# Kernel tuning notes

Hardware: AMD Instinct MI355X
Metric: run time of the kernel (lower is better)

Reference implementation:

```python
import jax, jax.numpy as jnp
import numpy as np

B, LQ, LKV, D, H = 4, 1024, 4096, 512, 4
HD = D // H  # head dim = 128


def setup_inputs() -> dict:
    key = jax.random.key(0)
    ks = jax.random.split(key, 6)
    s = 1.0 / np.sqrt(D)
    return {
        "x": jax.random.normal(ks[0], (B, LQ, D), jnp.float32),
        "encoder_feats": jax.random.normal(ks[1], (B, LKV, D), jnp.float32),
        "Wq": jax.random.normal(ks[2], (D, D), jnp.float32) * s,
        "Wk": jax.random.normal(ks[3], (D, D), jnp.float32) * s,
        "Wv": jax.random.normal(ks[4], (D, D), jnp.float32) * s,
        "bq": jnp.zeros((D,), jnp.float32),
        "bk": jnp.zeros((D,), jnp.float32),
        "bv": jnp.zeros((D,), jnp.float32),
        "Wo": jax.random.normal(ks[5], (D, D), jnp.float32) * s,
        "bo": jnp.zeros((D,), jnp.float32),
    }


def reference(x, encoder_feats, Wq, Wk, Wv, bq, bk, bv, Wo, bo):
    # nn.MultiheadAttention explicit (non-flash) path, dropout=0, eval.
    # Project, split heads: [B, L, D] -> [B, H, L, HD]
    def heads(t, L):
        return t.reshape(B, L, H, HD).transpose(0, 2, 1, 3)

    q = heads(x @ Wq.T + bq, LQ)
    k = heads(encoder_feats @ Wk.T + bk, LKV)
    v = heads(encoder_feats @ Wv.T + bv, LKV)

    scale = 1.0 / jnp.sqrt(jnp.asarray(HD, x.dtype))
    scores = jnp.einsum("bhqd,bhkd->bhqk", q, k) * scale  # [B,H,LQ,LKV]
    attn = jax.nn.softmax(scores, axis=-1)
    ctx = jnp.einsum("bhqk,bhkd->bhqd", attn, v)  # [B,H,LQ,HD]
    ctx = ctx.transpose(0, 2, 1, 3).reshape(B, LQ, D)
    attn_output = ctx @ Wo.T + bo
    # forward() returns attn_output only (fused/LayerNorm result is discarded)
    return attn_output
```

## Files before the change

kernel.cpp:

```cpp
#include <hip/hip_runtime.h>
#include <math.h>

#define B_    4
#define LQ_   1024
#define LKV_  4096
#define DM    512
#define NH    4
#define HD_   128

typedef _Float16 half8   __attribute__((ext_vector_type(8)));
typedef _Float16 half4_t __attribute__((ext_vector_type(4)));
typedef float    floatx4 __attribute__((ext_vector_type(4)));

#define MFMA16(a, b, c) __builtin_amdgcn_mfma_f32_16x16x32_f16((a), (b), (c), 0, 0, 0)

#define SWZ(c, r) ((c) ^ (((r) & 7) << 3))

__global__ __launch_bounds__(256) void prep_w(
    const float* __restrict__ Wq, const float* __restrict__ Wk,
    const float* __restrict__ Wv, const float* __restrict__ Wo,
    _Float16* __restrict__ Wh)
{
  int i = blockIdx.x * 256 + threadIdx.x;
  int wsel = i >> 16;
  const float* src = (wsel == 0) ? Wq : (wsel == 1) ? Wk : (wsel == 2) ? Wv : Wo;
  size_t off = i & 65535;
  float4 v = *(const float4*)(src + off * 4);
  half4_t h;
  h[0] = (_Float16)v.x; h[1] = (_Float16)v.y;
  h[2] = (_Float16)v.z; h[3] = (_Float16)v.w;
  *(half4_t*)(Wh + ((size_t)wsel << 18) + off * 4) = h;
}

__global__ __launch_bounds__(256, 2) void proj_qkv(
    const float* __restrict__ x,
    const float* __restrict__ enc,
    const _Float16* __restrict__ Whq,
    const _Float16* __restrict__ Whk,
    const _Float16* __restrict__ Whv,
    const float* __restrict__ bq,
    const float* __restrict__ bk,
    const float* __restrict__ bv,
    _Float16* __restrict__ Qh,
    _Float16* __restrict__ Kh,
    _Float16* __restrict__ Vt,
    float qscale)
{
  __shared__ _Float16 SM[3 * 128 * 72];
  _Float16 (*Xs)[72]  = (_Float16(*)[72])SM;
  _Float16 (*Ws1)[72] = (_Float16(*)[72])(SM + 128 * 72);
  _Float16 (*Ws2)[72] = (_Float16(*)[72])(SM + 2 * 128 * 72);

  const int tid  = threadIdx.x;
  const int lane = tid & 63;
  const int w    = tid >> 6;
  const int n16  = lane & 15;
  const int quad = lane >> 4;
  const int wm   = (w & 1) * 64;
  const int wn   = (w >> 1) * 64;
  const int col0 = blockIdx.y * 128;

  if ((int)blockIdx.x >= 128) {
    const int row0 = ((int)blockIdx.x - 128) * 128;
    floatx4 acc[4][4];
#pragma unroll
    for (int a = 0; a < 4; ++a)
#pragma unroll
      for (int b = 0; b < 4; ++b) acc[a][b] = (floatx4){0.f, 0.f, 0.f, 0.f};

    for (int k0 = 0; k0 < 512; k0 += 64) {
#pragma unroll
      for (int i = 0; i < 4; ++i) {
        int c = i * 256 + tid;
        int r = c >> 3, off = (c & 7) * 8;
        const float* xp = x + (size_t)(row0 + r) * 512 + k0 + off;
        float4 a = *(const float4*)xp, b2 = *(const float4*)(xp + 4);
        half8 hx;
        hx[0] = (_Float16)a.x;  hx[1] = (_Float16)a.y;
        hx[2] = (_Float16)a.z;  hx[3] = (_Float16)a.w;
        hx[4] = (_Float16)b2.x; hx[5] = (_Float16)b2.y;
        hx[6] = (_Float16)b2.z; hx[7] = (_Float16)b2.w;
        *(half8*)&Xs[r][off] = hx;
        *(half8*)&Ws1[r][off] = *(const half8*)(Whq + (size_t)(col0 + r) * 512 + k0 + off);
      }
      __syncthreads();
#pragma unroll
      for (int kc = 0; kc < 2; ++kc) {
        half8 af[4], bf[4];
#pragma unroll
        for (int mb = 0; mb < 4; ++mb)
          af[mb] = *(const half8*)&Xs[wm + mb * 16 + n16][kc * 32 + quad * 8];
#pragma unroll
        for (int nb = 0; nb < 4; ++nb)
          bf[nb] = *(const half8*)&Ws1[wn + nb * 16 + n16][kc * 32 + quad * 8];
#pragma unroll
        for (int mb = 0; mb < 4; ++mb)
#pragma unroll
          for (int nb = 0; nb < 4; ++nb)
            acc[mb][nb] = MFMA16(af[mb], bf[nb], acc[mb][nb]);
      }
      __syncthreads();
    }
#pragma unroll
    for (int mb = 0; mb < 4; ++mb)
#pragma unroll
      for (int nb = 0; nb < 4; ++nb)
#pragma unroll
        for (int r = 0; r < 4; ++r) {
          int row = row0 + wm + mb * 16 + quad * 4 + r;
          int col = col0 + wn + nb * 16 + n16;
          Qh[(size_t)row * 512 + col] =
              (_Float16)((acc[mb][nb][r] + bq[col]) * qscale);
        }
    return;
  }

  const int row0 = (int)blockIdx.x * 128;
  floatx4 accK[4][4], accV[4][4];
#pragma unroll
  for (int a = 0; a < 4; ++a)
#pragma unroll
    for (int b = 0; b < 4; ++b) {
      accK[a][b] = (floatx4){0.f, 0.f, 0.f, 0.f};
      accV[a][b] = (floatx4){0.f, 0.f, 0.f, 0.f};
    }

  for (int k0 = 0; k0 < 512; k0 += 64) {
#pragma unroll
    for (int i = 0; i < 4; ++i) {
      int c = i * 256 + tid;
      int r = c >> 3, off = (c & 7) * 8;
      const float* xp = enc + (size_t)(row0 + r) * 512 + k0 + off;
      float4 a = *(const float4*)xp, b2 = *(const float4*)(xp + 4);
      half8 hx;
      hx[0] = (_Float16)a.x;  hx[1] = (_Float16)a.y;
      hx[2] = (_Float16)a.z;  hx[3] = (_Float16)a.w;
      hx[4] = (_Float16)b2.x; hx[5] = (_Float16)b2.y;
      hx[6] = (_Float16)b2.z; hx[7] = (_Float16)b2.w;
      *(half8*)&Xs[r][off] = hx;
      *(half8*)&Ws1[r][off] = *(const half8*)(Whk + (size_t)(col0 + r) * 512 + k0 + off);
      *(half8*)&Ws2[r][off] = *(const half8*)(Whv + (size_t)(col0 + r) * 512 + k0 + off);
    }
    __syncthreads();
#pragma unroll
    for (int kc = 0; kc < 2; ++kc) {
      half8 af[4], bkf[4], bvf[4];
#pragma unroll
      for (int mb = 0; mb < 4; ++mb)
        af[mb] = *(const half8*)&Xs[wm + mb * 16 + n16][kc * 32 + quad * 8];
#pragma unroll
      for (int nb = 0; nb < 4; ++nb) {
        bkf[nb] = *(const half8*)&Ws1[wn + nb * 16 + n16][kc * 32 + quad * 8];
        bvf[nb] = *(const half8*)&Ws2[wn + nb * 16 + n16][kc * 32 + quad * 8];
      }
#pragma unroll
      for (int mb = 0; mb < 4; ++mb)
#pragma unroll
        for (int nb = 0; nb < 4; ++nb) {
          accK[mb][nb] = MFMA16(af[mb], bkf[nb], accK[mb][nb]);
          accV[mb][nb] = MFMA16(af[mb], bvf[nb], accV[mb][nb]);
        }
    }
    __syncthreads();
  }

#pragma unroll
  for (int mb = 0; mb < 4; ++mb)
#pragma unroll
    for (int nb = 0; nb < 4; ++nb)
#pragma unroll
      for (int r = 0; r < 4; ++r) {
        int row = row0 + wm + mb * 16 + quad * 4 + r;
        int col = col0 + wn + nb * 16 + n16;
        Kh[(size_t)row * 512 + col] = (_Float16)(accK[mb][nb][r] + bk[col]);
      }

  _Float16 (*Ts)[144] = (_Float16(*)[144])SM;
#pragma unroll
  for (int mb = 0; mb < 4; ++mb)
#pragma unroll
    for (int nb = 0; nb < 4; ++nb) {
      int dl = wn + nb * 16 + n16;
      float bi = bv[col0 + dl];
      half4_t hv;
#pragma unroll
      for (int r = 0; r < 4; ++r) hv[r] = (_Float16)(accV[mb][nb][r] + bi);
      *(half4_t*)&Ts[dl][wm + mb * 16 + quad * 4] = hv;
    }
  __syncthreads();
  int b   = row0 >> 12;
  int kv0 = row0 & 4095;
#pragma unroll
  for (int i = 0; i < 8; ++i) {
    int f = i * 256 + tid;
    int dl = f >> 4, kv8 = (f & 15) * 8;
    half8 ov = *(const half8*)&Ts[dl][kv8];
    *(half8*)(Vt + (size_t)((b * 4 + blockIdx.y) * 128 + dl) * LKV_ + kv0 + kv8) = ov;
  }
}

__global__ __launch_bounds__(256, 2) void flash_mfma2(
    const _Float16* __restrict__ Qh,
    const _Float16* __restrict__ Kh,
    const _Float16* __restrict__ Vtg,
    _Float16* __restrict__ Opart,
    float* __restrict__ ml)
{
  __shared__ _Float16 U[64 * 128];
  __shared__ _Float16 Vs[128 * 64];
  _Float16* Ks = U;
  _Float16* Ps = U;

  const int tid  = threadIdx.x;
  const int lane = tid & 63;
  const int w    = tid >> 6;
  const int n16  = lane & 15;
  const int quad = lane >> 4;

  const int xb    = blockIdx.x;
  const int qt    = blockIdx.y;
  const int split = xb & 3;
  const int bh    = xb >> 2;
  const int h = bh & 3, b = bh >> 2;

  const _Float16* Qg = Qh + (size_t)(b * LQ_ + qt * 128) * DM + h * HD_;
  const _Float16* Kg = Kh + (size_t)(b * LKV_) * DM + h * HD_;
  const _Float16* Vg = Vtg + (size_t)(bh * HD_) * LKV_;

  half8 qf[2][4];
  const int chunk = w >> 1;
  const int qrb   = (w & 1) * 32;
#pragma unroll
  for (int c = 0; c < 2; ++c) {
#pragma unroll
    for (int i = 0; i < 4; ++i) {
      int f = i * 256 + tid;
      int r = f >> 4, c8 = (f & 15) * 8;
      *(half8*)&Ks[r * 128 + SWZ(c8, r)] =
          *(const half8*)(Qg + (size_t)(c * 64 + r) * DM + c8);
    }
    __syncthreads();
    if (chunk == c) {
#pragma unroll
      for (int qb = 0; qb < 2; ++qb) {
        int qr = qrb + qb * 16 + n16;
#pragma unroll
        for (int kc = 0; kc < 4; ++kc)
          qf[qb][kc] = *(const half8*)&Ks[qr * 128 + SWZ(kc * 32 + quad * 8, qr)];
      }
    }
    __syncthreads();
  }

  floatx4 o[2][8];
#pragma unroll
  for (int mb = 0; mb < 2; ++mb)
#pragma unroll
    for (int vb = 0; vb < 8; ++vb) o[mb][vb] = (floatx4){0.f, 0.f, 0.f, 0.f};
  float m_i[2] = {-INFINITY, -INFINITY};
  float l_i[2] = {0.f, 0.f};

  for (int kt = split * 16; kt < split * 16 + 16; ++kt) {
#pragma unroll
    for (int i = 0; i < 4; ++i) {
      int f = i * 256 + tid;
      int r = f >> 4, c8 = (f & 15) * 8;
      *(half8*)&Ks[r * 128 + SWZ(c8, r)] =
          *(const half8*)(Kg + (size_t)(kt * 64 + r) * DM + c8);
    }
#pragma unroll
    for (int i = 0; i < 4; ++i) {
      int f = i * 256 + tid;
      int d = f >> 3, kv8 = (f & 7) * 8;
      *(half8*)&Vs[d * 64 + SWZ(kv8, d)] =
          *(const half8*)(Vg + (size_t)d * LKV_ + kt * 64 + kv8);
    }
    __syncthreads();

    floatx4 s[2][4];
#pragma unroll
    for (int qb = 0; qb < 2; ++qb)
#pragma unroll
      for (int cb = 0; cb < 4; ++cb) s[qb][cb] = (floatx4){0.f, 0.f, 0.f, 0.f};
#pragma unroll
    for (int cb = 0; cb < 4; ++cb) {
      int kr = cb * 16 + n16;
#pragma unroll
      for (int kc = 0; kc < 4; ++kc) {
        half8 kf = *(const half8*)&Ks[kr * 128 + SWZ(kc * 32 + quad * 8, kr)];
        s[0][cb] = MFMA16(kf, qf[0][kc], s[0][cb]);
        s[1][cb] = MFMA16(kf, qf[1][kc], s[1][cb]);
      }
    }
    __syncthreads();

    float alpha[2];
#pragma unroll
    for (int qb = 0; qb < 2; ++qb) {
      float mx = -INFINITY;
#pragma unroll
      for (int cb = 0; cb < 4; ++cb)
#pragma unroll
        for (int r = 0; r < 4; ++r) mx = fmaxf(mx, s[qb][cb][r]);
      mx = fmaxf(mx, __shfl_xor(mx, 16));
      mx = fmaxf(mx, __shfl_xor(mx, 32));
      float mn = fmaxf(m_i[qb], mx);
      alpha[qb] = __expf(m_i[qb] - mn);
      m_i[qb] = mn;
      float rs = 0.f;
      int pr = w * 32 + qb * 16 + n16;
#pragma unroll
      for (int cb = 0; cb < 4; ++cb) {
        half4_t ph;
#pragma unroll
        for (int r = 0; r < 4; ++r) {
          float p = __expf(s[qb][cb][r] - mn);
          rs += p;
          ph[r] = (_Float16)p;
        }
        *(half4_t*)&Ps[pr * 64 + SWZ(cb * 16 + quad * 4, pr)] = ph;
      }
      rs += __shfl_xor(rs, 16);
      rs += __shfl_xor(rs, 32);
      l_i[qb] = l_i[qb] * alpha[qb] + rs;
    }

    if (__ballot((alpha[0] != 1.f) || (alpha[1] != 1.f))) {
#pragma unroll
      for (int mb = 0; mb < 2; ++mb) {
#pragma unroll
        for (int r = 0; r < 4; ++r) {
          float a = __shfl(alpha[mb], (lane & 48) | (quad * 4 + r));
#pragma unroll
          for (int vb = 0; vb < 8; ++vb) o[mb][vb][r] *= a;
        }
      }
    }

    half8 pf[2][2];
#pragma unroll
    for (int mb = 0; mb < 2; ++mb) {
      int pr = w * 32 + mb * 16 + n16;
#pragma unroll
      for (int kc = 0; kc < 2; ++kc)
        pf[mb][kc] = *(const half8*)&Ps[pr * 64 + SWZ(kc * 32 + quad * 8, pr)];
    }
#pragma unroll
    for (int vb = 0; vb < 8; ++vb) {
      int vr = vb * 16 + n16;
#pragma unroll
      for (int kc = 0; kc < 2; ++kc) {
        half8 vf = *(const half8*)&Vs[vr * 64 + SWZ(kc * 32 + quad * 8, vr)];
        o[0][vb] = MFMA16(pf[0][kc], vf, o[0][vb]);
        o[1][vb] = MFMA16(pf[1][kc], vf, o[1][vb]);
      }
    }
    __syncthreads();
  }

  _Float16* Og = Opart + ((size_t)xb * 1024 + qt * 128 + w * 32) * HD_;
#pragma unroll
  for (int mb = 0; mb < 2; ++mb)
#pragma unroll
    for (int r = 0; r < 4; ++r)
#pragma unroll
      for (int vb = 0; vb < 8; ++vb)
        Og[(size_t)(mb * 16 + quad * 4 + r) * HD_ + vb * 16 + n16] =
            (_Float16)o[mb][vb][r];
  if (quad == 0) {
#pragma unroll
    for (int qb = 0; qb < 2; ++qb) {
      size_t qi = (size_t)xb * 1024 + qt * 128 + w * 32 + qb * 16 + n16;
      ml[qi * 2] = m_i[qb];
      ml[qi * 2 + 1] = l_i[qb];
    }
  }
}

__global__ __launch_bounds__(256) void proj_out_fused(
    const _Float16* __restrict__ Opart,
    const float* __restrict__ ml,
    const _Float16* __restrict__ Who,
    const float* __restrict__ bo,
    float* __restrict__ Y)
{
  __shared__ _Float16 Xs[64][72];
  __shared__ _Float16 Ws[128][72];
  __shared__ float CW[4][64][8];

  const int tid  = threadIdx.x;
  const int lane = tid & 63;
  const int w    = tid >> 6;
  const int n16  = lane & 15;
  const int quad = lane >> 4;
  const int wm   = (w & 1) * 32;
  const int wn   = (w >> 1) * 64;
  const int row0 = blockIdx.x * 64;
  const int col0 = blockIdx.y * 128;
  const int b    = row0 >> 10;

  {
    int h = tid >> 6, r = tid & 63;
    int q = (row0 + r) & 1023;
    int bh = b * 4 + h;
    float m[4], l[4], M = -INFINITY;
#pragma unroll
    for (int p = 0; p < 4; ++p) {
      size_t idx = ((size_t)(bh * 4 + p) * 1024 + q) * 2;
      m[p] = ml[idx]; l[p] = ml[idx + 1];
      M = fmaxf(M, m[p]);
    }
    float L = 0.f, wts[4];
#pragma unroll
    for (int p = 0; p < 4; ++p) { wts[p] = __expf(m[p] - M); L += wts[p] * l[p]; }
    float inv = 1.f / L;
#pragma unroll
    for (int p = 0; p < 4; ++p) CW[h][r][p] = wts[p] * inv;
    CW[h][r][4] = 0.f;
  }
  __syncthreads();

  floatx4 acc[2][4];
#pragma unroll
  for (int a = 0; a < 2; ++a)
#pragma unroll
    for (int c = 0; c < 4; ++c) acc[a][c] = (floatx4){0.f, 0.f, 0.f, 0.f};

  for (int k0 = 0; k0 < 512; k0 += 64) {
    int h = k0 >> 7, d0 = k0 & 127;
    int bh = b * 4 + h;
#pragma unroll
    for (int i = 0; i < 2; ++i) {
      int f = i * 256 + tid;
      int r = f >> 3, c8 = (f & 7) * 8;
      int q = (row0 + r) & 1023;
      float w0 = CW[h][r][0], w1 = CW[h][r][1];
      float w2 = CW[h][r][2], w3 = CW[h][r][3];
      size_t base = ((size_t)(bh * 4) * 1024 + q) * 128 + d0 + c8;
      half8 v0 = *(const half8*)(Opart + base);
      half8 v1 = *(const half8*)(Opart + base + 131072);
      half8 v2 = *(const half8*)(Opart + base + 262144);
      half8 v3 = *(const half8*)(Opart + base + 393216);
      half8 hx;
#pragma unroll
      for (int j = 0; j < 8; ++j)
        hx[j] = (_Float16)(w0 * (float)v0[j] + w1 * (float)v1[j] +
                           w2 * (float)v2[j] + w3 * (float)v3[j]);
      *(half8*)&Xs[r][c8] = hx;
    }
#pragma unroll
    for (int i = 0; i < 4; ++i) {
      int f = i * 256 + tid;
      int r = f >> 3, c8 = (f & 7) * 8;
      *(half8*)&Ws[r][c8] = *(const half8*)(Who + (size_t)(col0 + r) * 512 + k0 + c8);
    }
    __syncthreads();
#pragma unroll
    for (int kc = 0; kc < 2; ++kc) {
      half8 af[2], bf[4];
#pragma unroll
      for (int mb = 0; mb < 2; ++mb)
        af[mb] = *(const half8*)&Xs[wm + mb * 16 + n16][kc * 32 + quad * 8];
#pragma unroll
      for (int nb = 0; nb < 4; ++nb)
        bf[nb] = *(const half8*)&Ws[wn + nb * 16 + n16][kc * 32 + quad * 8];
#pragma unroll
      for (int mb = 0; mb < 2; ++mb)
#pragma unroll
        for (int nb = 0; nb < 4; ++nb)
          acc[mb][nb] = MFMA16(af[mb], bf[nb], acc[mb][nb]);
    }
    __syncthreads();
  }

#pragma unroll
  for (int mb = 0; mb < 2; ++mb)
#pragma unroll
    for (int nb = 0; nb < 4; ++nb)
#pragma unroll
      for (int r = 0; r < 4; ++r) {
        int row = row0 + wm + mb * 16 + quad * 4 + r;
        int col = col0 + wn + nb * 16 + n16;
        Y[(size_t)row * 512 + col] = acc[mb][nb][r] + bo[col];
      }
}

extern "C" void kernel_launch(void* const* d_in, const int* in_sizes, int n_in,
                              void* d_out, int out_size, void* d_ws, size_t ws_size,
                              hipStream_t stream) {
  const float* x   = (const float*)d_in[0];
  const float* enc = (const float*)d_in[1];
  const float* Wq  = (const float*)d_in[2];
  const float* Wk  = (const float*)d_in[3];
  const float* Wv  = (const float*)d_in[4];
  const float* bq  = (const float*)d_in[5];
  const float* bk  = (const float*)d_in[6];
  const float* bv  = (const float*)d_in[7];
  const float* Wo  = (const float*)d_in[8];
  const float* bo  = (const float*)d_in[9];
  float* out = (float*)d_out;

  char* ws = (char*)d_ws;
  _Float16* Qh    = (_Float16*)(ws);
  _Float16* Kh    = (_Float16*)(ws + (4u  << 20));
  _Float16* Vtg   = (_Float16*)(ws + (20u << 20));
  _Float16* Opart = (_Float16*)(ws + (36u << 20));
  float*    mlp   = (float*)   (ws + (52u << 20));
  _Float16* Wh    = (_Float16*)(ws + (53u << 20));

  _Float16* Whq = Wh;
  _Float16* Whk = Wh + 262144;
  _Float16* Whv = Wh + 524288;
  _Float16* Who = Wh + 786432;

  const float qscale = 0.08838834764831845f;
  dim3 blk(256);

  prep_w<<<dim3(1024), blk, 0, stream>>>(Wq, Wk, Wv, Wo, Wh);

  proj_qkv<<<dim3(160, 4), blk, 0, stream>>>(
      x, enc, Whq, Whk, Whv, bq, bk, bv, Qh, Kh, Vtg, qscale);

  flash_mfma2<<<dim3(64, 8), blk, 0, stream>>>(Qh, Kh, Vtg, Opart, mlp);

  proj_out_fused<<<dim3(64, 4), blk, 0, stream>>>(Opart, mlp, Who, bo, out);
}
```

Before: 205.8 us.

## Swizzle GEMM shared tiles and transpose flash PV accumulator for coalesced stores

Replaces the padded 72-wide shared tiles in the projection and output GEMM kernels with unpadded 64-wide tiles using XOR swizzle, cutting LDS footprint while still avoiding bank conflicts. In the flash kernel the PV MFMA operands are swapped so the accumulator is held transposed; the alpha rescale then becomes a plain per-lane multiply with no shuffles. The output is staged through shared memory and written with coalesced 16-byte stores instead of scattered 2-byte stores. The staging adds an extra barrier and LDS round trip at the end of the flash kernel.

New measurement: 193.5 us. -6.0%, faster.

```diff
diff --git a/kernel.cpp b/kernel.cpp
--- a/kernel.cpp
+++ b/kernel.cpp
@@ -46,10 +46,10 @@
     _Float16* __restrict__ Vt,
     float qscale)
 {
-  __shared__ _Float16 SM[3 * 128 * 72];
-  _Float16 (*Xs)[72]  = (_Float16(*)[72])SM;
-  _Float16 (*Ws1)[72] = (_Float16(*)[72])(SM + 128 * 72);
-  _Float16 (*Ws2)[72] = (_Float16(*)[72])(SM + 2 * 128 * 72);
+  __shared__ _Float16 SM[3 * 128 * 64];
+  _Float16* Xs  = SM;
+  _Float16* Ws1 = SM + 128 * 64;
+  _Float16* Ws2 = SM + 2 * 128 * 64;
 
   const int tid  = threadIdx.x;
   const int lane = tid & 63;
@@ -80,19 +80,24 @@
         hx[2] = (_Float16)a.z;  hx[3] = (_Float16)a.w;
         hx[4] = (_Float16)b2.x; hx[5] = (_Float16)b2.y;
         hx[6] = (_Float16)b2.z; hx[7] = (_Float16)b2.w;
-        *(half8*)&Xs[r][off] = hx;
-        *(half8*)&Ws1[r][off] = *(const half8*)(Whq + (size_t)(col0 + r) * 512 + k0 + off);
+        *(half8*)&Xs[r * 64 + SWZ(off, r)] = hx;
+        *(half8*)&Ws1[r * 64 + SWZ(off, r)] =
+            *(const half8*)(Whq + (size_t)(col0 + r) * 512 + k0 + off);
       }
       __syncthreads();
 #pragma unroll
       for (int kc = 0; kc < 2; ++kc) {
         half8 af[4], bf[4];
 #pragma unroll
-        for (int mb = 0; mb < 4; ++mb)
-          af[mb] = *(const half8*)&Xs[wm + mb * 16 + n16][kc * 32 + quad * 8];
-#pragma unroll
-        for (int nb = 0; nb < 4; ++nb)
-          bf[nb] = *(const half8*)&Ws1[wn + nb * 16 + n16][kc * 32 + quad * 8];
+        for (int mb = 0; mb < 4; ++mb) {
+          int r = wm + mb * 16 + n16;
+          af[mb] = *(const half8*)&Xs[r * 64 + SWZ(kc * 32 + quad * 8, r)];
+        }
+#pragma unroll
+        for (int nb = 0; nb < 4; ++nb) {
+          int r = wn + nb * 16 + n16;
+          bf[nb] = *(const half8*)&Ws1[r * 64 + SWZ(kc * 32 + quad * 8, r)];
+        }
 #pragma unroll
         for (int mb = 0; mb < 4; ++mb)
 #pragma unroll
@@ -137,21 +142,26 @@
       hx[2] = (_Float16)a.z;  hx[3] = (_Float16)a.w;
       hx[4] = (_Float16)b2.x; hx[5] = (_Float16)b2.y;
       hx[6] = (_Float16)b2.z; hx[7] = (_Float16)b2.w;
-      *(half8*)&Xs[r][off] = hx;
-      *(half8*)&Ws1[r][off] = *(const half8*)(Whk + (size_t)(col0 + r) * 512 + k0 + off);
-      *(half8*)&Ws2[r][off] = *(const half8*)(Whv + (size_t)(col0 + r) * 512 + k0 + off);
+      *(half8*)&Xs[r * 64 + SWZ(off, r)] = hx;
+      *(half8*)&Ws1[r * 64 + SWZ(off, r)] =
+          *(const half8*)(Whk + (size_t)(col0 + r) * 512 + k0 + off);
+      *(half8*)&Ws2[r * 64 + SWZ(off, r)] =
+          *(const half8*)(Whv + (size_t)(col0 + r) * 512 + k0 + off);
     }
     __syncthreads();
 #pragma unroll
     for (int kc = 0; kc < 2; ++kc) {
       half8 af[4], bkf[4], bvf[4];
 #pragma unroll
-      for (int mb = 0; mb < 4; ++mb)
-        af[mb] = *(const half8*)&Xs[wm + mb * 16 + n16][kc * 32 + quad * 8];
+      for (int mb = 0; mb < 4; ++mb) {
+        int r = wm + mb * 16 + n16;
+        af[mb] = *(const half8*)&Xs[r * 64 + SWZ(kc * 32 + quad * 8, r)];
+      }
 #pragma unroll
       for (int nb = 0; nb < 4; ++nb) {
-        bkf[nb] = *(const half8*)&Ws1[wn + nb * 16 + n16][kc * 32 + quad * 8];
-        bvf[nb] = *(const half8*)&Ws2[wn + nb * 16 + n16][kc * 32 + quad * 8];
+        int r = wn + nb * 16 + n16;
+        bkf[nb] = *(const half8*)&Ws1[r * 64 + SWZ(kc * 32 + quad * 8, r)];
+        bvf[nb] = *(const half8*)&Ws2[r * 64 + SWZ(kc * 32 + quad * 8, r)];
       }
 #pragma unroll
       for (int mb = 0; mb < 4; ++mb)
@@ -206,10 +216,10 @@
     _Float16* __restrict__ Opart,
     float* __restrict__ ml)
 {
-  __shared__ _Float16 U[64 * 128];
-  __shared__ _Float16 Vs[128 * 64];
-  _Float16* Ks = U;
-  _Float16* Ps = U;
+  __shared__ _Float16 SH[2 * 64 * 128];
+  _Float16* Ks = SH;
+  _Float16* Ps = SH;
+  _Float16* Vs = SH + 64 * 128;
 
   const int tid  = threadIdx.x;
   const int lane = tid & 63;
@@ -252,11 +262,11 @@
     __syncthreads();
   }
 
-  floatx4 o[2][8];
-#pragma unroll
-  for (int mb = 0; mb < 2; ++mb)
-#pragma unroll
-    for (int vb = 0; vb < 8; ++vb) o[mb][vb] = (floatx4){0.f, 0.f, 0.f, 0.f};
+  floatx4 oT[2][8];
+#pragma unroll
+  for (int qb = 0; qb < 2; ++qb)
+#pragma unroll
+    for (int vb = 0; vb < 8; ++vb) oT[qb][vb] = (floatx4){0.f, 0.f, 0.f, 0.f};
   float m_i[2] = {-INFINITY, -INFINITY};
   float l_i[2] = {0.f, 0.f};
 
@@ -327,23 +337,19 @@
 
     if (__ballot((alpha[0] != 1.f) || (alpha[1] != 1.f))) {
 #pragma unroll
-      for (int mb = 0; mb < 2; ++mb) {
-#pragma unroll
-        for (int r = 0; r < 4; ++r) {
-          float a = __shfl(alpha[mb], (lane & 48) | (quad * 4 + r));
-#pragma unroll
-          for (int vb = 0; vb < 8; ++vb) o[mb][vb][r] *= a;
-        }
-      }
+      for (int qb = 0; qb < 2; ++qb)
+#pragma unroll
+        for (int vb = 0; vb < 8; ++vb)
+          oT[qb][vb] *= alpha[qb];
     }
 
     half8 pf[2][2];
 #pragma unroll
-    for (int mb = 0; mb < 2; ++mb) {
-      int pr = w * 32 + mb * 16 + n16;
+    for (int qb = 0; qb < 2; ++qb) {
+      int pr = w * 32 + qb * 16 + n16;
 #pragma unroll
       for (int kc = 0; kc < 2; ++kc)
-        pf[mb][kc] = *(const half8*)&Ps[pr * 64 + SWZ(kc * 32 + quad * 8, pr)];
+        pf[qb][kc] = *(const half8*)&Ps[pr * 64 + SWZ(kc * 32 + quad * 8, pr)];
     }
 #pragma unroll
     for (int vb = 0; vb < 8; ++vb) {
@@ -351,22 +357,33 @@
 #pragma unroll
       for (int kc = 0; kc < 2; ++kc) {
         half8 vf = *(const half8*)&Vs[vr * 64 + SWZ(kc * 32 + quad * 8, vr)];
-        o[0][vb] = MFMA16(pf[0][kc], vf, o[0][vb]);
-        o[1][vb] = MFMA16(pf[1][kc], vf, o[1][vb]);
-      }
-    }
-    __syncthreads();
-  }
-
-  _Float16* Og = Opart + ((size_t)xb * 1024 + qt * 128 + w * 32) * HD_;
-#pragma unroll
-  for (int mb = 0; mb < 2; ++mb)
-#pragma unroll
-    for (int r = 0; r < 4; ++r)
-#pragma unroll
-      for (int vb = 0; vb < 8; ++vb)
-        Og[(size_t)(mb * 16 + quad * 4 + r) * HD_ + vb * 16 + n16] =
-            (_Float16)o[mb][vb][r];
+        oT[0][vb] = MFMA16(vf, pf[0][kc], oT[0][vb]);
+        oT[1][vb] = MFMA16(vf, pf[1][kc], oT[1][vb]);
+      }
+    }
+    __syncthreads();
+  }
+
+  _Float16* Os = SH;
+#pragma unroll
+  for (int qb = 0; qb < 2; ++qb) {
+    int q = w * 32 + qb * 16 + n16;
+#pragma unroll
+    for (int vb = 0; vb < 8; ++vb) {
+      half4_t hv;
+#pragma unroll
+      for (int r = 0; r < 4; ++r) hv[r] = (_Float16)oT[qb][vb][r];
+      *(half4_t*)&Os[q * 128 + SWZ(vb * 16 + quad * 4, q)] = hv;
+    }
+  }
+  __syncthreads();
+  _Float16* Og = Opart + ((size_t)xb * 1024 + qt * 128) * HD_;
+#pragma unroll
+  for (int i = 0; i < 8; ++i) {
+    int f = i * 256 + tid;
+    int q = f >> 4, c8 = (f & 15) * 8;
+    *(half8*)(Og + (size_t)q * HD_ + c8) = *(const half8*)&Os[q * 128 + SWZ(c8, q)];
+  }
   if (quad == 0) {
 #pragma unroll
     for (int qb = 0; qb < 2; ++qb) {
@@ -384,8 +401,8 @@
     const float* __restrict__ bo,
     float* __restrict__ Y)
 {
-  __shared__ _Float16 Xs[64][72];
-  __shared__ _Float16 Ws[128][72];
+  __shared__ _Float16 Xs[64 * 64];
+  __shared__ _Float16 Ws[128 * 64];
   __shared__ float CW[4][64][8];
 
   const int tid  = threadIdx.x;
@@ -416,7 +433,6 @@
     float inv = 1.f / L;
 #pragma unroll
     for (int p = 0; p < 4; ++p) CW[h][r][p] = wts[p] * inv;
-    CW[h][r][4] = 0.f;
   }
   __syncthreads();
 
@@ -446,24 +462,29 @@
       for (int j = 0; j < 8; ++j)
         hx[j] = (_Float16)(w0 * (float)v0[j] + w1 * (float)v1[j] +
                            w2 * (float)v2[j] + w3 * (float)v3[j]);
-      *(half8*)&Xs[r][c8] = hx;
+      *(half8*)&Xs[r * 64 + SWZ(c8, r)] = hx;
     }
 #pragma unroll
     for (int i = 0; i < 4; ++i) {
       int f = i * 256 + tid;
       int r = f >> 3, c8 = (f & 7) * 8;
-      *(half8*)&Ws[r][c8] = *(const half8*)(Who + (size_t)(col0 + r) * 512 + k0 + c8);
+      *(half8*)&Ws[r * 64 + SWZ(c8, r)] =
+          *(const half8*)(Who + (size_t)(col0 + r) * 512 + k0 + c8);
     }
     __syncthreads();
 #pragma unroll
     for (int kc = 0; kc < 2; ++kc) {
       half8 af[2], bf[4];
 #pragma unroll
-      for (int mb = 0; mb < 2; ++mb)
-        af[mb] = *(const half8*)&Xs[wm + mb * 16 + n16][kc * 32 + quad * 8];
-#pragma unroll
-      for (int nb = 0; nb < 4; ++nb)
-        bf[nb] = *(const half8*)&Ws[wn + nb * 16 + n16][kc * 32 + quad * 8];
+      for (int mb = 0; mb < 2; ++mb) {
+        int r = wm + mb * 16 + n16;
+        af[mb] = *(const half8*)&Xs[r * 64 + SWZ(kc * 32 + quad * 8, r)];
+      }
+#pragma unroll
+      for (int nb = 0; nb < 4; ++nb) {
+        int r = wn + nb * 16 + n16;
+        bf[nb] = *(const half8*)&Ws[r * 64 + SWZ(kc * 32 + quad * 8, r)];
+      }
 #pragma unroll
       for (int mb = 0; mb < 2; ++mb)
 #pragma unroll
```
